# Kernel optimization log

Hardware: AMD Instinct MI355X
Metric: run time of the kernel (lower is better)

## Reference

```python
import jax, jax.numpy as jnp
import numpy as np

N_USERS = 50000
N_ENTITIES = 100000
N_FACTORS = 8
N_RELATIONS = 17  # weight has n_relations-1 = 16 rows
EMB = 64
N_EDGES = 2_000_000
NNZ = 2_000_000
SLOPE = 0.2


def setup_inputs() -> dict:
    key = jax.random.key(0)
    ks = jax.random.split(key, 16)
    inp = {
        "entity_emb": jax.random.normal(ks[0], (N_ENTITIES, EMB), jnp.float32),
        "user_emb": jax.random.normal(ks[1], (N_USERS, EMB), jnp.float32),
        "latent_emb": jax.random.normal(ks[2], (N_FACTORS, EMB), jnp.float32),
        "edge_index": jax.random.randint(ks[3], (2, N_EDGES), 0, N_ENTITIES, jnp.int32),
        "edge_type": jax.random.randint(ks[4], (N_EDGES,), 1, N_RELATIONS, jnp.int32),
        "interact_rows": jax.random.randint(ks[5], (NNZ,), 0, N_USERS, jnp.int32),
        "interact_cols": jax.random.randint(ks[6], (NNZ,), 0, N_ENTITIES, jnp.int32),
        "interact_vals": jax.random.uniform(ks[7], (NNZ,), jnp.float32),
        "weight": jax.random.normal(ks[8], (N_RELATIONS - 1, EMB), jnp.float32),
        "entity_cate_set": jax.random.randint(ks[9], (N_ENTITIES,), 1, 33, jnp.int32),
        # params (torch Linear convention: y = x @ W.T + b)
        "W_user_att": jax.random.normal(ks[10], (N_FACTORS, N_FACTORS), jnp.float32) * 0.1,
        "b_user_att": jnp.zeros((N_FACTORS,), jnp.float32),
        "W_weight_att": jax.random.normal(ks[11], (N_RELATIONS - 1, N_RELATIONS - 1), jnp.float32) * 0.1,
        "b_weight_att": jnp.zeros((N_RELATIONS - 1,), jnp.float32),
        "W1": jax.random.normal(ks[12], (EMB, EMB), jnp.float32) * 0.1,
        "b1": jnp.zeros((EMB,), jnp.float32),
        "W2": jax.random.normal(ks[13], (EMB, EMB), jnp.float32) * 0.1,
        "b2": jnp.zeros((EMB,), jnp.float32),
    }
    return inp


def _lin(x, W, b):
    return x @ W.T + b


def reference(entity_emb, user_emb, latent_emb, edge_index, edge_type,
              interact_rows, interact_cols, interact_vals, weight, entity_cate_set,
              W_user_att, b_user_att, W_weight_att, b_weight_att, W1, b1, W2, b2):
    head, tail = edge_index[0], edge_index[1]

    # KG aggregate: gather-multiply-scatter_mean (is_div=False branch)
    neigh = entity_emb[tail] * weight[edge_type - 1]            # [E, C]
    sums = jax.ops.segment_sum(neigh, head, num_segments=N_ENTITIES)
    cnt = jax.ops.segment_sum(jnp.ones((neigh.shape[0],), neigh.dtype),
                              head, num_segments=N_ENTITIES)
    entity_agg = sums / jnp.maximum(cnt, 1.0)[:, None]          # [N_ent, C]

    # user aggregate: sparse mm (COO) interact_mat @ entity_emb
    user_agg = jax.ops.segment_sum(interact_vals[:, None] * entity_emb[interact_cols],
                                   interact_rows, num_segments=N_USERS)  # [U, C]

    # user -> latent interest attention
    score_ = _lin(user_emb, W1, b1) @ _lin(latent_emb, W1, b1).T          # [U, F]
    score = jax.nn.softmax(jax.nn.leaky_relu(_lin(score_, W_user_att, b_user_att), SLOPE), axis=1)  # [U, F]

    score_rp = _lin(latent_emb, W2, b2) @ _lin(weight, W2, b2).T          # [F, R-1]
    latent_new = jax.nn.softmax(jax.nn.leaky_relu(_lin(score_rp, W_weight_att, b_weight_att), SLOPE), axis=-1) @ weight  # [F, C]

    # (disen_weight * score).sum(dim=1) == score @ latent_new
    user_agg = user_agg * (score @ latent_new) + user_agg
    return (entity_agg, user_agg, latent_new)
```

## Files before the change

kernel.cpp:

```cpp
#include <hip/hip_runtime.h>
#include <hip/hip_bf16.h>

#define N_USERS    50000
#define N_ENTITIES 100000
#define EMB        64
#define N_EDGES    2000000
#define NNZ        2000000
#define SLOPE      0.2f

#define KROWS   256
#define KSHIFT  8
#define NBK     391
#define UROWS   128
#define USHIFT  7
#define NBU     391
#define CAPK    8192
#define CAPU    7680
#define CHUNK   8192
#define PB      ((N_EDGES + CHUNK - 1) / CHUNK)

__global__ __launch_bounds__(512) void hist_both(const int* __restrict__ head,
                                                 const int* __restrict__ urows,
                                                 int* __restrict__ kgOffs,
                                                 int* __restrict__ uOffs) {
    __shared__ int lhk[NBK];
    __shared__ int lhu[NBU];
    int tid = threadIdx.x;
    for (int t = tid; t < NBK; t += 512) lhk[t] = 0;
    for (int t = tid; t < NBU; t += 512) lhu[t] = 0;
    __syncthreads();
    int base = blockIdx.x * CHUNK;
#pragma unroll 4
    for (int j = 0; j < CHUNK / 512; ++j) {
        int i = base + j * 512 + tid;
        if (i < N_EDGES) atomicAdd(&lhk[head[i] >> KSHIFT], 1);
        if (i < NNZ)     atomicAdd(&lhu[urows[i] >> USHIFT], 1);
    }
    __syncthreads();
    for (int t = tid; t < NBK; t += 512) { int c = lhk[t]; if (c) atomicAdd(&kgOffs[t], c); }
    for (int t = tid; t < NBU; t += 512) { int c = lhu[t]; if (c) atomicAdd(&uOffs[t], c); }
}

__global__ __launch_bounds__(512) void scan_both(int* __restrict__ kgOffs,
                                                 int* __restrict__ kgCur,
                                                 int* __restrict__ uOffs,
                                                 int* __restrict__ uCur) {
    __shared__ int tsum[512];
    int n     = (blockIdx.x == 0) ? NBK : NBU;
    int* offs = (blockIdx.x == 0) ? kgOffs : uOffs;
    int* cur  = (blockIdx.x == 0) ? kgCur  : uCur;
    int tid = threadIdx.x;
    int v = (tid < n) ? offs[tid] : 0;
    tsum[tid] = v;
    __syncthreads();
    for (int off = 1; off < 512; off <<= 1) {
        int t = (tid >= off) ? tsum[tid - off] : 0;
        __syncthreads();
        tsum[tid] += t;
        __syncthreads();
    }
    if (tid < n) { int e = tsum[tid] - v; offs[tid] = e; cur[tid] = e; }
    if (tid == n - 1) offs[n] = tsum[tid];
}

__global__ __launch_bounds__(512) void scatter_both(const int* __restrict__ head,
                                                    const int* __restrict__ tail,
                                                    const int* __restrict__ etype,
                                                    int* __restrict__ kgCur,
                                                    int* __restrict__ kgPay,
                                                    const int* __restrict__ urows,
                                                    const int* __restrict__ ucols,
                                                    const float* __restrict__ uvals,
                                                    int* __restrict__ uCur,
                                                    int2* __restrict__ uPay) {
    __shared__ int lh[NBK];
    __shared__ int lb[NBK];
    int tid = threadIdx.x;
    bool isKg = blockIdx.x < PB;
    int base = (isKg ? blockIdx.x : blockIdx.x - PB) * CHUNK;

    for (int t = tid; t < NBK; t += 512) lh[t] = 0;
    __syncthreads();
    if (isKg) {
#pragma unroll 4
        for (int j = 0; j < CHUNK / 512; ++j) {
            int i = base + j * 512 + tid;
            if (i < N_EDGES) atomicAdd(&lh[head[i] >> KSHIFT], 1);
        }
    } else {
#pragma unroll 4
        for (int j = 0; j < CHUNK / 512; ++j) {
            int i = base + j * 512 + tid;
            if (i < NNZ) atomicAdd(&lh[urows[i] >> USHIFT], 1);
        }
    }
    __syncthreads();
    int* cur = isKg ? kgCur : uCur;
    for (int t = tid; t < NBK; t += 512) {
        int c = lh[t];
        lb[t] = c ? atomicAdd(&cur[t], c) : 0;
        lh[t] = 0;
    }
    __syncthreads();
    if (isKg) {
#pragma unroll 4
        for (int j = 0; j < CHUNK / 512; ++j) {
            int i = base + j * 512 + tid;
            if (i < N_EDGES) {
                int h = head[i];
                int b = h >> KSHIFT;
                int p = lb[b] + atomicAdd(&lh[b], 1);
                kgPay[p] = tail[i] | ((etype[i] - 1) << 17) | ((h & (KROWS - 1)) << 21);
            }
        }
    } else {
#pragma unroll 4
        for (int j = 0; j < CHUNK / 512; ++j) {
            int i = base + j * 512 + tid;
            if (i < NNZ) {
                int r = urows[i];
                int b = r >> USHIFT;
                int p = lb[b] + atomicAdd(&lh[b], 1);
                uPay[p] = make_int2(ucols[i] | ((r & (UROWS - 1)) << 17),
                                    __float_as_int(uvals[i]));
            }
        }
    }
}

__global__ __launch_bounds__(1024, 8) void acc_both(
        const int* __restrict__ kgPay, const int* __restrict__ kgOffs,
        const int2* __restrict__ uPay, const int* __restrict__ uOffs,
        const float* __restrict__ entity_emb,
        const float* __restrict__ weight,
        const float* __restrict__ user_emb,
        const float* __restrict__ P,
        const float* __restrict__ cvec,
        const float* __restrict__ W_user_att,
        const float* __restrict__ b_user_att,
        const float* __restrict__ latent_new,
        float* __restrict__ ent_out,
        float* __restrict__ user_out) {
    __shared__ long long smem8[7873];
    int t = threadIdx.x, d = t & 63, wv = t >> 6;

    if (blockIdx.x < NBK) {
        int* spay = (int*)smem8;
        int* lcnt = spay + CAPK;
        int* lofs = lcnt + KROWS;
        int* sc   = lofs + KROWS + 1;
        int start = kgOffs[blockIdx.x], end = kgOffs[blockIdx.x + 1];
        int n = end - start; if (n > CAPK) n = CAPK;

        if (t < KROWS) lcnt[t] = 0;
        __syncthreads();
        for (int i = t; i < n; i += 1024)
            atomicAdd(&lcnt[(kgPay[start + i] >> 21) & (KROWS - 1)], 1);
        __syncthreads();
        if (t < KROWS) sc[t] = lcnt[t];
        __syncthreads();
        for (int off = 1; off < KROWS; off <<= 1) {
            int v = (t < KROWS && t >= off) ? sc[t - off] : 0;
            __syncthreads();
            if (t < KROWS) sc[t] += v;
            __syncthreads();
        }
        if (t < KROWS) { int e = sc[t] - lcnt[t]; lofs[t] = e; lcnt[t] = e; }
        if (t == 0) lofs[KROWS] = n;
        __syncthreads();
        for (int i = t; i < n; i += 1024) {
            int v = kgPay[start + i];
            int p = atomicAdd(&lcnt[(v >> 21) & (KROWS - 1)], 1);
            spay[p] = v;
        }
        __syncthreads();

        int rowbase = blockIdx.x * KROWS;
        for (int rr = 0; rr < KROWS / 16; ++rr) {
            int r = wv * (KROWS / 16) + rr;
            int gr = rowbase + r;
            if (gr >= N_ENTITIES) break;
            int s0 = lofs[r], e0 = lofs[r + 1];
            int cnt = e0 - s0;
            float acc = 0.f;
            int i = s0;
            for (; i + 7 < e0; i += 8) {
                float a0 = 0.f, a1 = 0.f;
#pragma unroll
                for (int u = 0; u < 8; u += 2) {
                    int va = spay[i + u], vb = spay[i + u + 1];
                    a0 += entity_emb[(va & 0x1FFFF) * EMB + d] * weight[((va >> 17) & 15) * EMB + d];
                    a1 += entity_emb[(vb & 0x1FFFF) * EMB + d] * weight[((vb >> 17) & 15) * EMB + d];
                }
                acc += a0 + a1;
            }
            for (; i < e0; ++i) {
                int v = spay[i];
                acc += entity_emb[(v & 0x1FFFF) * EMB + d] * weight[((v >> 17) & 15) * EMB + d];
            }
            for (int j = start + CAPK; j < end; ++j) {
                int v = kgPay[j];
                if (((v >> 21) & (KROWS - 1)) == r) {
                    acc += entity_emb[(v & 0x1FFFF) * EMB + d] * weight[((v >> 17) & 15) * EMB + d];
                    ++cnt;
                }
            }
            ent_out[gr * EMB + d] = acc / fmaxf((float)cnt, 1.f);
        }
    } else {
        int2* spay = (int2*)smem8;
        int* lcnt = (int*)(spay + CAPU);
        int* lofs = lcnt + UROWS;
        int* sc   = lofs + UROWS + 1;
        int bk = blockIdx.x - NBK;
        int start = uOffs[bk], end = uOffs[bk + 1];
        int n = end - start; if (n > CAPU) n = CAPU;

        if (t < UROWS) lcnt[t] = 0;
        __syncthreads();
        for (int i = t; i < n; i += 1024)
            atomicAdd(&lcnt[(uPay[start + i].x >> 17) & (UROWS - 1)], 1);
        __syncthreads();
        if (t < UROWS) sc[t] = lcnt[t];
        __syncthreads();
        for (int off = 1; off < UROWS; off <<= 1) {
            int v = (t < UROWS && t >= off) ? sc[t - off] : 0;
            __syncthreads();
            if (t < UROWS) sc[t] += v;
            __syncthreads();
        }
        if (t < UROWS) { int e = sc[t] - lcnt[t]; lofs[t] = e; lcnt[t] = e; }
        if (t == 0) lofs[UROWS] = n;
        __syncthreads();
        for (int i = t; i < n; i += 1024) {
            int2 v = uPay[start + i];
            int p = atomicAdd(&lcnt[(v.x >> 17) & (UROWS - 1)], 1);
            spay[p] = v;
        }
        __syncthreads();

        int rowbase = bk * UROWS;
        for (int rr = 0; rr < UROWS / 16; ++rr) {
            int r = wv * (UROWS / 16) + rr;
            int gr = rowbase + r;
            if (gr >= N_USERS) break;
            int s0 = lofs[r], e0 = lofs[r + 1];
            float acc = 0.f;
            int i = s0;
            for (; i + 7 < e0; i += 8) {
                float a0 = 0.f, a1 = 0.f;
#pragma unroll
                for (int u = 0; u < 8; u += 2) {
                    int2 va = spay[i + u], vb = spay[i + u + 1];
                    a0 += __int_as_float(va.y) * entity_emb[(va.x & 0x1FFFF) * EMB + d];
                    a1 += __int_as_float(vb.y) * entity_emb[(vb.x & 0x1FFFF) * EMB + d];
                }
                acc += a0 + a1;
            }
            for (; i < e0; ++i) {
                int2 v = spay[i];
                acc += __int_as_float(v.y) * entity_emb[(v.x & 0x1FFFF) * EMB + d];
            }
            for (int j = start + CAPU; j < end; ++j) {
                int2 v = uPay[j];
                if (((v.x >> 17) & (UROWS - 1)) == r)
                    acc += __int_as_float(v.y) * entity_emb[(v.x & 0x1FFFF) * EMB + d];
            }

            float ue = user_emb[gr * EMB + d];
            float s[8];
#pragma unroll
            for (int f = 0; f < 8; ++f) s[f] = ue * P[d * 8 + f];
#pragma unroll
            for (int off = 32; off; off >>= 1) {
#pragma unroll
                for (int f = 0; f < 8; ++f) s[f] += __shfl_xor(s[f], off, 64);
            }
#pragma unroll
            for (int f = 0; f < 8; ++f) s[f] += cvec[f];
            float att[8];
            float mx = -1e30f;
#pragma unroll
            for (int k = 0; k < 8; ++k) {
                float a = b_user_att[k];
#pragma unroll
                for (int j = 0; j < 8; ++j) a += s[j] * W_user_att[k * 8 + j];
                a = a > 0.f ? a : SLOPE * a;
                att[k] = a;
                mx = fmaxf(mx, a);
            }
            float sum = 0.f;
#pragma unroll
            for (int k = 0; k < 8; ++k) { att[k] = __expf(att[k] - mx); sum += att[k]; }
            float inv = 1.f / sum;
            float g = 0.f;
#pragma unroll
            for (int f = 0; f < 8; ++f) g += att[f] * inv * latent_new[f * EMB + d];
            user_out[gr * EMB + d] = acc * (1.f + g);
        }
    }
}

__global__ void small_dense(const float* __restrict__ latent_emb,
                            const float* __restrict__ weight,
                            const float* __restrict__ W_weight_att,
                            const float* __restrict__ b_weight_att,
                            const float* __restrict__ W1,
                            const float* __restrict__ b1,
                            const float* __restrict__ W2,
                            const float* __restrict__ b2,
                            float* __restrict__ P_out,
                            float* __restrict__ c_out,
                            float* __restrict__ latent_new_out) {
    __shared__ float lat1[8 * 64];
    __shared__ float lat2[8 * 64];
    __shared__ float wl2[16 * 64];
    __shared__ float srp[8 * 16];
    __shared__ float soft[8 * 16];
    int l = threadIdx.x;

    for (int f = 0; f < 8; ++f) {
        float a1 = b1[l], a2 = b2[l];
        for (int k = 0; k < 64; ++k) {
            float le = latent_emb[f * 64 + k];
            a1 += le * W1[l * 64 + k];
            a2 += le * W2[l * 64 + k];
        }
        lat1[f * 64 + l] = a1;
        lat2[f * 64 + l] = a2;
    }
    for (int r = 0; r < 16; ++r) {
        float a = b2[l];
        for (int k = 0; k < 64; ++k) a += weight[r * 64 + k] * W2[l * 64 + k];
        wl2[r * 64 + l] = a;
    }
    __syncthreads();

    for (int f = 0; f < 8; ++f) {
        float p = 0.f;
        for (int d = 0; d < 64; ++d) p += W1[d * 64 + l] * lat1[f * 64 + d];
        P_out[l * 8 + f] = p;
    }
    if (l < 8) {
        float cc = 0.f;
        for (int d = 0; d < 64; ++d) cc += b1[d] * lat1[l * 64 + d];
        c_out[l] = cc;
    }
    for (int idx = l; idx < 128; idx += 64) {
        int f = idx >> 4, r = idx & 15;
        float a = 0.f;
        for (int d = 0; d < 64; ++d) a += lat2[f * 64 + d] * wl2[r * 64 + d];
        srp[idx] = a;
    }
    __syncthreads();

    if (l < 8) {
        int f = l;
        float att[16];
        float mx = -1e30f;
        for (int k = 0; k < 16; ++k) {
            float a = b_weight_att[k];
            for (int j = 0; j < 16; ++j) a += srp[f * 16 + j] * W_weight_att[k * 16 + j];
            a = a > 0.f ? a : SLOPE * a;
            att[k] = a;
            mx = fmaxf(mx, a);
        }
        float s = 0.f;
        for (int k = 0; k < 16; ++k) { att[k] = expf(att[k] - mx); s += att[k]; }
        float inv = 1.f / s;
        for (int k = 0; k < 16; ++k) soft[f * 16 + k] = att[k] * inv;
    }
    __syncthreads();

    for (int f = 0; f < 8; ++f) {
        float a = 0.f;
        for (int r = 0; r < 16; ++r) a += soft[f * 16 + r] * weight[r * 64 + l];
        latent_new_out[f * 64 + l] = a;
    }
}

__global__ void kg_scatter(const int* __restrict__ head, const int* __restrict__ tail,
                           const int* __restrict__ etype,
                           const float* __restrict__ entity_emb,
                           const float* __restrict__ weight,
                           float* __restrict__ sums, float* __restrict__ cnt) {
    int gid = blockIdx.x * blockDim.x + threadIdx.x;
    int e = gid >> 6, d = threadIdx.x & 63;
    if (e >= N_EDGES) return;
    int h = head[e], t = tail[e], w = etype[e] - 1;
    float v = entity_emb[t * EMB + d] * weight[w * EMB + d];
    unsafeAtomicAdd(&sums[h * EMB + d], v);
    if (d == 0) unsafeAtomicAdd(&cnt[h], 1.0f);
}

__global__ void user_scatter(const int* __restrict__ rows, const int* __restrict__ cols,
                             const float* __restrict__ vals,
                             const float* __restrict__ entity_emb,
                             float* __restrict__ user_sums) {
    int gid = blockIdx.x * blockDim.x + threadIdx.x;
    int e = gid >> 6, d = threadIdx.x & 63;
    if (e >= NNZ) return;
    float v = vals[e] * entity_emb[cols[e] * EMB + d];
    unsafeAtomicAdd(&user_sums[rows[e] * EMB + d], v);
}

__global__ void entity_div(float* __restrict__ ent, const float* __restrict__ cnt) {
    int gid = blockIdx.x * blockDim.x + threadIdx.x;
    if (gid >= N_ENTITIES * EMB) return;
    float c = cnt[gid >> 6];
    ent[gid] = ent[gid] / fmaxf(c, 1.0f);
}

__global__ void user_finalize(const float* __restrict__ user_emb,
                              const float* __restrict__ P,
                              const float* __restrict__ c,
                              const float* __restrict__ W_user_att,
                              const float* __restrict__ b_user_att,
                              const float* __restrict__ latent_new,
                              float* __restrict__ user_out) {
    int gid = blockIdx.x * blockDim.x + threadIdx.x;
    int u = gid >> 6, lane = threadIdx.x & 63;
    if (u >= N_USERS) return;
    float ue = user_emb[u * 64 + lane];
    float s[8];
#pragma unroll
    for (int f = 0; f < 8; ++f) s[f] = ue * P[lane * 8 + f];
#pragma unroll
    for (int off = 32; off; off >>= 1)
#pragma unroll
        for (int f = 0; f < 8; ++f) s[f] += __shfl_xor(s[f], off, 64);
#pragma unroll
    for (int f = 0; f < 8; ++f) s[f] += c[f];
    float att[8], mx = -1e30f;
#pragma unroll
    for (int k = 0; k < 8; ++k) {
        float a = b_user_att[k];
#pragma unroll
        for (int j = 0; j < 8; ++j) a += s[j] * W_user_att[k * 8 + j];
        a = a > 0.f ? a : SLOPE * a;
        att[k] = a;
        mx = fmaxf(mx, a);
    }
    float sum = 0.f;
#pragma unroll
    for (int k = 0; k < 8; ++k) { att[k] = expf(att[k] - mx); sum += att[k]; }
    float inv = 1.f / sum, g = 0.f;
#pragma unroll
    for (int f = 0; f < 8; ++f) g += att[f] * inv * latent_new[f * 64 + lane];
    float ua = user_out[u * 64 + lane];
    user_out[u * 64 + lane] = ua * (1.f + g);
}

extern "C" void kernel_launch(void* const* d_in, const int* in_sizes, int n_in,
                              void* d_out, int out_size, void* d_ws, size_t ws_size,
                              hipStream_t stream) {
    const float* entity_emb   = (const float*)d_in[0];
    const float* user_emb     = (const float*)d_in[1];
    const float* latent_emb   = (const float*)d_in[2];
    const int*   edge_index   = (const int*)d_in[3];
    const int*   edge_type    = (const int*)d_in[4];
    const int*   irows        = (const int*)d_in[5];
    const int*   icols        = (const int*)d_in[6];
    const float* ivals        = (const float*)d_in[7];
    const float* weight       = (const float*)d_in[8];
    const float* W_user_att   = (const float*)d_in[10];
    const float* b_user_att   = (const float*)d_in[11];
    const float* W_weight_att = (const float*)d_in[12];
    const float* b_weight_att = (const float*)d_in[13];
    const float* W1           = (const float*)d_in[14];
    const float* b1           = (const float*)d_in[15];
    const float* W2           = (const float*)d_in[16];
    const float* b2           = (const float*)d_in[17];

    float* out      = (float*)d_out;
    float* ent_out  = out;
    float* user_out = out + (size_t)N_ENTITIES * EMB;
    float* lat_out  = user_out + (size_t)N_USERS * EMB;

    const int* head = edge_index;
    const int* tail = edge_index + N_EDGES;

    int* ws_i = (int*)d_ws;
    int*   kgOffs = ws_i;
    int*   uOffs  = kgOffs + (NBK + 1);
    int*   kgCur  = uOffs + (NBU + 1);
    int*   uCur   = kgCur + NBK;
    int*   kgPay  = uCur + NBU;
    int2*  uPay   = (int2*)(kgPay + N_EDGES);
    float* Pbuf   = (float*)(uPay + NNZ);
    float* cbuf   = Pbuf + 64 * 8;
    size_t need_bytes = (size_t)((NBK + 1) + (NBU + 1) + NBK + NBU +
                                 N_EDGES + 2 * (size_t)NNZ + 512 + 8) * 4;

    if (ws_size >= need_bytes) {
        hipMemsetAsync(kgOffs, 0, (size_t)((NBK + 1) + (NBU + 1)) * sizeof(int), stream);

        hist_both<<<PB, 512, 0, stream>>>(head, irows, kgOffs, uOffs);
        scan_both<<<2, 512, 0, stream>>>(kgOffs, kgCur, uOffs, uCur);
        scatter_both<<<2 * PB, 512, 0, stream>>>(head, tail, edge_type, kgCur, kgPay,
                                                 irows, icols, ivals, uCur, uPay);
        small_dense<<<1, 64, 0, stream>>>(latent_emb, weight, W_weight_att,
                                          b_weight_att, W1, b1, W2, b2,
                                          Pbuf, cbuf, lat_out);
        acc_both<<<NBK + NBU, 1024, 0, stream>>>(kgPay, kgOffs, uPay, uOffs,
                                                 entity_emb, weight, user_emb,
                                                 Pbuf, cbuf, W_user_att, b_user_att,
                                                 lat_out, ent_out, user_out);
    } else {
        float* cnt   = (float*)d_ws;
        float* Pbuf2 = cnt + N_ENTITIES;
        float* cbuf2 = Pbuf2 + 64 * 8;
        hipMemsetAsync(ent_out, 0,
                       (size_t)(N_ENTITIES + N_USERS) * EMB * sizeof(float), stream);
        hipMemsetAsync(cnt, 0, N_ENTITIES * sizeof(float), stream);
        int blocks_edges = (N_EDGES * 64) / 256;
        kg_scatter<<<blocks_edges, 256, 0, stream>>>(head, tail, edge_type, entity_emb,
                                                     weight, ent_out, cnt);
        user_scatter<<<blocks_edges, 256, 0, stream>>>(irows, icols, ivals, entity_emb,
                                                       user_out);
        small_dense<<<1, 64, 0, stream>>>(latent_emb, weight, W_weight_att,
                                          b_weight_att, W1, b1, W2, b2,
                                          Pbuf2, cbuf2, lat_out);
        user_finalize<<<(N_USERS * 64) / 256, 256, 0, stream>>>(user_emb, Pbuf2, cbuf2,
                                                                W_user_att, b_user_att,
                                                                lat_out, user_out);
        entity_div<<<(N_ENTITIES * EMB) / 256, 256, 0, stream>>>(ent_out, cnt);
    }
}
```

Before: 442.4 us.

## Accumulate bucketed rows in shared-memory atomics instead of per-row local sort

```diff
diff --git a/kernel.cpp b/kernel.cpp
--- a/kernel.cpp
+++ b/kernel.cpp
@@ -1,5 +1,4 @@
 #include <hip/hip_runtime.h>
-#include <hip/hip_bf16.h>
 
 #define N_USERS    50000
 #define N_ENTITIES 100000
@@ -8,15 +7,12 @@
 #define NNZ        2000000
 #define SLOPE      0.2f
 
-#define KROWS   256
-#define KSHIFT  8
-#define NBK     391
-#define UROWS   128
-#define USHIFT  7
+#define RSHIFT  7
+#define BROWS   128
+#define NBK     782
 #define NBU     391
-#define CAPK    8192
-#define CAPU    7680
 #define CHUNK   8192
+#define EPT     (CHUNK / 512)
 #define PB      ((N_EDGES + CHUNK - 1) / CHUNK)
 
 __global__ __launch_bounds__(512) void hist_both(const int* __restrict__ head,
@@ -31,21 +27,21 @@
     __syncthreads();
     int base = blockIdx.x * CHUNK;
 #pragma unroll 4
-    for (int j = 0; j < CHUNK / 512; ++j) {
+    for (int j = 0; j < EPT; ++j) {
         int i = base + j * 512 + tid;
-        if (i < N_EDGES) atomicAdd(&lhk[head[i] >> KSHIFT], 1);
-        if (i < NNZ)     atomicAdd(&lhu[urows[i] >> USHIFT], 1);
+        if (i < N_EDGES) atomicAdd(&lhk[head[i] >> RSHIFT], 1);
+        if (i < NNZ)     atomicAdd(&lhu[urows[i] >> RSHIFT], 1);
     }
     __syncthreads();
     for (int t = tid; t < NBK; t += 512) { int c = lhk[t]; if (c) atomicAdd(&kgOffs[t], c); }
     for (int t = tid; t < NBU; t += 512) { int c = lhu[t]; if (c) atomicAdd(&uOffs[t], c); }
 }
 
-__global__ __launch_bounds__(512) void scan_both(int* __restrict__ kgOffs,
-                                                 int* __restrict__ kgCur,
-                                                 int* __restrict__ uOffs,
-                                                 int* __restrict__ uCur) {
-    __shared__ int tsum[512];
+__global__ __launch_bounds__(1024) void scan_both(int* __restrict__ kgOffs,
+                                                  int* __restrict__ kgCur,
+                                                  int* __restrict__ uOffs,
+                                                  int* __restrict__ uCur) {
+    __shared__ int tsum[1024];
     int n     = (blockIdx.x == 0) ? NBK : NBU;
     int* offs = (blockIdx.x == 0) ? kgOffs : uOffs;
     int* cur  = (blockIdx.x == 0) ? kgCur  : uCur;
@@ -53,7 +49,7 @@
     int v = (tid < n) ? offs[tid] : 0;
     tsum[tid] = v;
     __syncthreads();
-    for (int off = 1; off < 512; off <<= 1) {
+    for (int off = 1; off < 1024; off <<= 1) {
         int t = (tid >= off) ? tsum[tid - off] : 0;
         __syncthreads();
         tsum[tid] += t;
@@ -61,6 +57,105 @@
     }
     if (tid < n) { int e = tsum[tid] - v; offs[tid] = e; cur[tid] = e; }
     if (tid == n - 1) offs[n] = tsum[tid];
+}
+
+__device__ void small_dense_body(int l,
+                                 const float* __restrict__ latent_emb,
+                                 const float* __restrict__ weight,
+                                 const float* __restrict__ W_weight_att,
+                                 const float* __restrict__ b_weight_att,
+                                 const float* __restrict__ W1,
+                                 const float* __restrict__ b1,
+                                 const float* __restrict__ W2,
+                                 const float* __restrict__ b2,
+                                 float* __restrict__ P_out,
+                                 float* __restrict__ c_out,
+                                 float* __restrict__ latent_new_out) {
+    __shared__ float lat1[8 * 64];
+    __shared__ float lat2[8 * 64];
+    __shared__ float wl2[16 * 64];
+    __shared__ float srp[8 * 16];
+    __shared__ float soft[8 * 16];
+
+    if (l < 64) {
+        for (int f = 0; f < 8; ++f) {
+            float a1 = b1[l], a2 = b2[l];
+            for (int k = 0; k < 64; ++k) {
+                float le = latent_emb[f * 64 + k];
+                a1 += le * W1[l * 64 + k];
+                a2 += le * W2[l * 64 + k];
+            }
+            lat1[f * 64 + l] = a1;
+            lat2[f * 64 + l] = a2;
+        }
+        for (int r = 0; r < 16; ++r) {
+            float a = b2[l];
+            for (int k = 0; k < 64; ++k) a += weight[r * 64 + k] * W2[l * 64 + k];
+            wl2[r * 64 + l] = a;
+        }
+    }
+    __syncthreads();
+
+    if (l < 64) {
+        for (int f = 0; f < 8; ++f) {
+            float p = 0.f;
+            for (int d = 0; d < 64; ++d) p += W1[d * 64 + l] * lat1[f * 64 + d];
+            P_out[l * 8 + f] = p;
+        }
+        if (l < 8) {
+            float cc = 0.f;
+            for (int d = 0; d < 64; ++d) cc += b1[d] * lat1[l * 64 + d];
+            c_out[l] = cc;
+        }
+        for (int idx = l; idx < 128; idx += 64) {
+            int f = idx >> 4, r = idx & 15;
+            float a = 0.f;
+            for (int d = 0; d < 64; ++d) a += lat2[f * 64 + d] * wl2[r * 64 + d];
+            srp[idx] = a;
+        }
+    }
+    __syncthreads();
+
+    if (l < 8) {
+        int f = l;
+        float att[16];
+        float mx = -1e30f;
+        for (int k = 0; k < 16; ++k) {
+            float a = b_weight_att[k];
+            for (int j = 0; j < 16; ++j) a += srp[f * 16 + j] * W_weight_att[k * 16 + j];
+            a = a > 0.f ? a : SLOPE * a;
+            att[k] = a;
+            mx = fmaxf(mx, a);
+        }
+        float s = 0.f;
+        for (int k = 0; k < 16; ++k) { att[k] = expf(att[k] - mx); s += att[k]; }
+        float inv = 1.f / s;
+        for (int k = 0; k < 16; ++k) soft[f * 16 + k] = att[k] * inv;
+    }
+    __syncthreads();
+
+    if (l < 64) {
+        for (int f = 0; f < 8; ++f) {
+            float a = 0.f;
+            for (int r = 0; r < 16; ++r) a += soft[f * 16 + r] * weight[r * 64 + l];
+            latent_new_out[f * 64 + l] = a;
+        }
+    }
+}
+
+__global__ void small_dense(const float* __restrict__ latent_emb,
+                            const float* __restrict__ weight,
+                            const float* __restrict__ W_weight_att,
+                            const float* __restrict__ b_weight_att,
+                            const float* __restrict__ W1,
+                            const float* __restrict__ b1,
+                            const float* __restrict__ W2,
+                            const float* __restrict__ b2,
+                            float* __restrict__ P_out,
+                            float* __restrict__ c_out,
+                            float* __restrict__ latent_new_out) {
+    small_dense_body(threadIdx.x, latent_emb, weight, W_weight_att, b_weight_att,
+                     W1, b1, W2, b2, P_out, c_out, latent_new_out);
 }
 
 __global__ __launch_bounds__(512) void scatter_both(const int* __restrict__ head,
@@ -72,56 +167,72 @@
                                                     const int* __restrict__ ucols,
                                                     const float* __restrict__ uvals,
                                                     int* __restrict__ uCur,
-                                                    int2* __restrict__ uPay) {
+                                                    int2* __restrict__ uPay,
+                                                    const float* __restrict__ latent_emb,
+                                                    const float* __restrict__ weight,
+                                                    const float* __restrict__ W_weight_att,
+                                                    const float* __restrict__ b_weight_att,
+                                                    const float* __restrict__ W1,
+                                                    const float* __restrict__ b1,
+                                                    const float* __restrict__ W2,
+                                                    const float* __restrict__ b2,
+                                                    float* __restrict__ Pbuf,
+                                                    float* __restrict__ cbuf,
+                                                    float* __restrict__ lat_out) {
+    if (blockIdx.x == 2 * PB) {
+        small_dense_body(threadIdx.x, latent_emb, weight, W_weight_att,
+                         b_weight_att, W1, b1, W2, b2, Pbuf, cbuf, lat_out);
+        return;
+    }
+
     __shared__ int lh[NBK];
     __shared__ int lb[NBK];
     int tid = threadIdx.x;
     bool isKg = blockIdx.x < PB;
     int base = (isKg ? blockIdx.x : blockIdx.x - PB) * CHUNK;
+    int nb   = isKg ? NBK : NBU;
+    int nTot = isKg ? N_EDGES : NNZ;
+    const int* src = isKg ? head : urows;
+    int* cur = isKg ? kgCur : uCur;
 
     for (int t = tid; t < NBK; t += 512) lh[t] = 0;
     __syncthreads();
-    if (isKg) {
-#pragma unroll 4
-        for (int j = 0; j < CHUNK / 512; ++j) {
-            int i = base + j * 512 + tid;
-            if (i < N_EDGES) atomicAdd(&lh[head[i] >> KSHIFT], 1);
-        }
-    } else {
-#pragma unroll 4
-        for (int j = 0; j < CHUNK / 512; ++j) {
-            int i = base + j * 512 + tid;
-            if (i < NNZ) atomicAdd(&lh[urows[i] >> USHIFT], 1);
-        }
-    }
-    __syncthreads();
-    int* cur = isKg ? kgCur : uCur;
-    for (int t = tid; t < NBK; t += 512) {
+
+    int hreg[EPT];
+#pragma unroll
+    for (int j = 0; j < EPT; ++j) {
+        int i = base + j * 512 + tid;
+        int h = (i < nTot) ? src[i] : -1;
+        hreg[j] = h;
+        if (h >= 0) atomicAdd(&lh[h >> RSHIFT], 1);
+    }
+    __syncthreads();
+    for (int t = tid; t < nb; t += 512) {
         int c = lh[t];
         lb[t] = c ? atomicAdd(&cur[t], c) : 0;
         lh[t] = 0;
     }
     __syncthreads();
     if (isKg) {
-#pragma unroll 4
-        for (int j = 0; j < CHUNK / 512; ++j) {
-            int i = base + j * 512 + tid;
-            if (i < N_EDGES) {
-                int h = head[i];
-                int b = h >> KSHIFT;
+#pragma unroll
+        for (int j = 0; j < EPT; ++j) {
+            int h = hreg[j];
+            if (h >= 0) {
+                int i = base + j * 512 + tid;
+                int b = h >> RSHIFT;
                 int p = lb[b] + atomicAdd(&lh[b], 1);
-                kgPay[p] = tail[i] | ((etype[i] - 1) << 17) | ((h & (KROWS - 1)) << 21);
+                kgPay[p] = tail[i] | ((etype[i] - 1) << 17) | ((h & (BROWS - 1)) << 21);
             }
         }
     } else {
-#pragma unroll 4
-        for (int j = 0; j < CHUNK / 512; ++j) {
-            int i = base + j * 512 + tid;
-            if (i < NNZ) {
-                int r = urows[i];
-                int b = r >> USHIFT;
+#pragma unroll
+        for (int j = 0; j < EPT; ++j) {
+            int h = hreg[j];
+            if (h >= 0) {
+                int i = base + j * 512 + tid;
+                int b = h >> RSHIFT;
                 int p = lb[b] + atomicAdd(&lh[b], 1);
-                uPay[p] = make_int2(ucols[i] | ((r & (UROWS - 1)) << 17),
+                uPay[p] = make_int2(ucols[i] | ((h & (BROWS - 1)) << 17),
                                     __float_as_int(uvals[i]));
             }
         }
@@ -141,136 +252,54 @@
         const float* __restrict__ latent_new,
         float* __restrict__ ent_out,
         float* __restrict__ user_out) {
-    __shared__ long long smem8[7873];
-    int t = threadIdx.x, d = t & 63, wv = t >> 6;
-
-    if (blockIdx.x < NBK) {
-        int* spay = (int*)smem8;
-        int* lcnt = spay + CAPK;
-        int* lofs = lcnt + KROWS;
-        int* sc   = lofs + KROWS + 1;
-        int start = kgOffs[blockIdx.x], end = kgOffs[blockIdx.x + 1];
-        int n = end - start; if (n > CAPK) n = CAPK;
-
-        if (t < KROWS) lcnt[t] = 0;
+    __shared__ float accum[BROWS * EMB];
+    __shared__ int   lcnt[BROWS];
+    int t  = threadIdx.x;
+    int wv = t >> 6, l = t & 63;
+    int h  = l >> 5, dd = l & 31;
+    int lane2 = (wv << 1) + h;
+
+    float4* a4 = (float4*)accum;
+    a4[t]        = make_float4(0.f, 0.f, 0.f, 0.f);
+    a4[t + 1024] = make_float4(0.f, 0.f, 0.f, 0.f);
+    if (t < BROWS) lcnt[t] = 0;
+    __syncthreads();
+
+    const float2* e2 = (const float2*)entity_emb;
+
+    if (blockIdx.x < NBU) {
+        int bk = blockIdx.x;
+        int start = uOffs[bk], n = uOffs[bk + 1] - start;
+        const int2* pay = uPay + start;
+        int nIt = (n + 31) >> 5;
+#pragma unroll 2
+        for (int it = 0; it < nIt; ++it) {
+            int ie = (it << 5) + lane2;
+            if (ie < n) {
+                int2 v = pay[ie];
+                int col = v.x & 0x1FFFF;
+                int r   = (v.x >> 17) & (BROWS - 1);
+                float val = __int_as_float(v.y);
+                float2 e = e2[(col << 5) + dd];
+                float p0 = val * e.x, p1 = val * e.y;
+                int wb = (r << 6) + (dd << 1);
+                atomicAdd(&accum[wb + h],       h ? p1 : p0);
+                atomicAdd(&accum[wb + (1 ^ h)], h ? p0 : p1);
+            }
+        }
         __syncthreads();
-        for (int i = t; i < n; i += 1024)
-            atomicAdd(&lcnt[(kgPay[start + i] >> 21) & (KROWS - 1)], 1);
-        __syncthreads();
-        if (t < KROWS) sc[t] = lcnt[t];
-        __syncthreads();
-        for (int off = 1; off < KROWS; off <<= 1) {
-            int v = (t < KROWS && t >= off) ? sc[t - off] : 0;
-            __syncthreads();
-            if (t < KROWS) sc[t] += v;
-            __syncthreads();
-        }
-        if (t < KROWS) { int e = sc[t] - lcnt[t]; lofs[t] = e; lcnt[t] = e; }
-        if (t == 0) lofs[KROWS] = n;
-        __syncthreads();
-        for (int i = t; i < n; i += 1024) {
-            int v = kgPay[start + i];
-            int p = atomicAdd(&lcnt[(v >> 21) & (KROWS - 1)], 1);
-            spay[p] = v;
-        }
-        __syncthreads();
-
-        int rowbase = blockIdx.x * KROWS;
-        for (int rr = 0; rr < KROWS / 16; ++rr) {
-            int r = wv * (KROWS / 16) + rr;
-            int gr = rowbase + r;
-            if (gr >= N_ENTITIES) break;
-            int s0 = lofs[r], e0 = lofs[r + 1];
-            int cnt = e0 - s0;
-            float acc = 0.f;
-            int i = s0;
-            for (; i + 7 < e0; i += 8) {
-                float a0 = 0.f, a1 = 0.f;
-#pragma unroll
-                for (int u = 0; u < 8; u += 2) {
-                    int va = spay[i + u], vb = spay[i + u + 1];
-                    a0 += entity_emb[(va & 0x1FFFF) * EMB + d] * weight[((va >> 17) & 15) * EMB + d];
-                    a1 += entity_emb[(vb & 0x1FFFF) * EMB + d] * weight[((vb >> 17) & 15) * EMB + d];
-                }
-                acc += a0 + a1;
-            }
-            for (; i < e0; ++i) {
-                int v = spay[i];
-                acc += entity_emb[(v & 0x1FFFF) * EMB + d] * weight[((v >> 17) & 15) * EMB + d];
-            }
-            for (int j = start + CAPK; j < end; ++j) {
-                int v = kgPay[j];
-                if (((v >> 21) & (KROWS - 1)) == r) {
-                    acc += entity_emb[(v & 0x1FFFF) * EMB + d] * weight[((v >> 17) & 15) * EMB + d];
-                    ++cnt;
-                }
-            }
-            ent_out[gr * EMB + d] = acc / fmaxf((float)cnt, 1.f);
-        }
-    } else {
-        int2* spay = (int2*)smem8;
-        int* lcnt = (int*)(spay + CAPU);
-        int* lofs = lcnt + UROWS;
-        int* sc   = lofs + UROWS + 1;
-        int bk = blockIdx.x - NBK;
-        int start = uOffs[bk], end = uOffs[bk + 1];
-        int n = end - start; if (n > CAPU) n = CAPU;
-
-        if (t < UROWS) lcnt[t] = 0;
-        __syncthreads();
-        for (int i = t; i < n; i += 1024)
-            atomicAdd(&lcnt[(uPay[start + i].x >> 17) & (UROWS - 1)], 1);
-        __syncthreads();
-        if (t < UROWS) sc[t] = lcnt[t];
-        __syncthreads();
-        for (int off = 1; off < UROWS; off <<= 1) {
-            int v = (t < UROWS && t >= off) ? sc[t - off] : 0;
-            __syncthreads();
-            if (t < UROWS) sc[t] += v;
-            __syncthreads();
-        }
-        if (t < UROWS) { int e = sc[t] - lcnt[t]; lofs[t] = e; lcnt[t] = e; }
-        if (t == 0) lofs[UROWS] = n;
-        __syncthreads();
-        for (int i = t; i < n; i += 1024) {
-            int2 v = uPay[start + i];
-            int p = atomicAdd(&lcnt[(v.x >> 17) & (UROWS - 1)], 1);
-            spay[p] = v;
-        }
-        __syncthreads();
-
-        int rowbase = bk * UROWS;
-        for (int rr = 0; rr < UROWS / 16; ++rr) {
-            int r = wv * (UROWS / 16) + rr;
+
+        int rowbase = bk * BROWS;
+        for (int k = 0; k < BROWS / 16; ++k) {
+            int r = (k << 4) + wv;
             int gr = rowbase + r;
             if (gr >= N_USERS) break;
-            int s0 = lofs[r], e0 = lofs[r + 1];
-            float acc = 0.f;
-            int i = s0;
-            for (; i + 7 < e0; i += 8) {
-                float a0 = 0.f, a1 = 0.f;
-#pragma unroll
-                for (int u = 0; u < 8; u += 2) {
-                    int2 va = spay[i + u], vb = spay[i + u + 1];
-                    a0 += __int_as_float(va.y) * entity_emb[(va.x & 0x1FFFF) * EMB + d];
-                    a1 += __int_as_float(vb.y) * entity_emb[(vb.x & 0x1FFFF) * EMB + d];
-                }
-                acc += a0 + a1;
-            }
-            for (; i < e0; ++i) {
-                int2 v = spay[i];
-                acc += __int_as_float(v.y) * entity_emb[(v.x & 0x1FFFF) * EMB + d];
-            }
-            for (int j = start + CAPU; j < end; ++j) {
-                int2 v = uPay[j];
-                if (((v.x >> 17) & (UROWS - 1)) == r)
-                    acc += __int_as_float(v.y) * entity_emb[(v.x & 0x1FFFF) * EMB + d];
-            }
-
-            float ue = user_emb[gr * EMB + d];
+            float acc = accum[(r << 6) + l];
+
+            float ue = user_emb[(size_t)gr * EMB + l];
             float s[8];
 #pragma unroll
-            for (int f = 0; f < 8; ++f) s[f] = ue * P[d * 8 + f];
+            for (int f = 0; f < 8; ++f) s[f] = ue * P[l * 8 + f];
 #pragma unroll
             for (int off = 32; off; off >>= 1) {
 #pragma unroll
@@ -281,101 +310,56 @@
             float att[8];
             float mx = -1e30f;
 #pragma unroll
-            for (int k = 0; k < 8; ++k) {
-                float a = b_user_att[k];
-#pragma unroll
-                for (int j = 0; j < 8; ++j) a += s[j] * W_user_att[k * 8 + j];
+            for (int q = 0; q < 8; ++q) {
+                float a = b_user_att[q];
+#pragma unroll
+                for (int j = 0; j < 8; ++j) a += s[j] * W_user_att[q * 8 + j];
                 a = a > 0.f ? a : SLOPE * a;
-                att[k] = a;
+                att[q] = a;
                 mx = fmaxf(mx, a);
             }
             float sum = 0.f;
 #pragma unroll
-            for (int k = 0; k < 8; ++k) { att[k] = __expf(att[k] - mx); sum += att[k]; }
+            for (int q = 0; q < 8; ++q) { att[q] = __expf(att[q] - mx); sum += att[q]; }
             float inv = 1.f / sum;
             float g = 0.f;
 #pragma unroll
-            for (int f = 0; f < 8; ++f) g += att[f] * inv * latent_new[f * EMB + d];
-            user_out[gr * EMB + d] = acc * (1.f + g);
-        }
-    }
-}
-
-__global__ void small_dense(const float* __restrict__ latent_emb,
-                            const float* __restrict__ weight,
-                            const float* __restrict__ W_weight_att,
-                            const float* __restrict__ b_weight_att,
-                            const float* __restrict__ W1,
-                            const float* __restrict__ b1,
-                            const float* __restrict__ W2,
-                            const float* __restrict__ b2,
-                            float* __restrict__ P_out,
-                            float* __restrict__ c_out,
-                            float* __restrict__ latent_new_out) {
-    __shared__ float lat1[8 * 64];
-    __shared__ float lat2[8 * 64];
-    __shared__ float wl2[16 * 64];
-    __shared__ float srp[8 * 16];
-    __shared__ float soft[8 * 16];
-    int l = threadIdx.x;
-
-    for (int f = 0; f < 8; ++f) {
-        float a1 = b1[l], a2 = b2[l];
-        for (int k = 0; k < 64; ++k) {
-            float le = latent_emb[f * 64 + k];
-            a1 += le * W1[l * 64 + k];
-            a2 += le * W2[l * 64 + k];
-        }
-        lat1[f * 64 + l] = a1;
-        lat2[f * 64 + l] = a2;
-    }
-    for (int r = 0; r < 16; ++r) {
-        float a = b2[l];
-        for (int k = 0; k < 64; ++k) a += weight[r * 64 + k] * W2[l * 64 + k];
-        wl2[r * 64 + l] = a;
-    }
-    __syncthreads();
-
-    for (int f = 0; f < 8; ++f) {
-        float p = 0.f;
-        for (int d = 0; d < 64; ++d) p += W1[d * 64 + l] * lat1[f * 64 + d];
-        P_out[l * 8 + f] = p;
-    }
-    if (l < 8) {
-        float cc = 0.f;
-        for (int d = 0; d < 64; ++d) cc += b1[d] * lat1[l * 64 + d];
-        c_out[l] = cc;
-    }
-    for (int idx = l; idx < 128; idx += 64) {
-        int f = idx >> 4, r = idx & 15;
-        float a = 0.f;
-        for (int d = 0; d < 64; ++d) a += lat2[f * 64 + d] * wl2[r * 64 + d];
-        srp[idx] = a;
-    }
-    __syncthreads();
-
-    if (l < 8) {
-        int f = l;
-        float att[16];
-        float mx = -1e30f;
-        for (int k = 0; k < 16; ++k) {
-            float a = b_weight_att[k];
-            for (int j = 0; j < 16; ++j) a += srp[f * 16 + j] * W_weight_att[k * 16 + j];
-            a = a > 0.f ? a : SLOPE * a;
-            att[k] = a;
-            mx = fmaxf(mx, a);
-        }
-        float s = 0.f;
-        for (int k = 0; k < 16; ++k) { att[k] = expf(att[k] - mx); s += att[k]; }
-        float inv = 1.f / s;
-        for (int k = 0; k < 16; ++k) soft[f * 16 + k] = att[k] * inv;
-    }
-    __syncthreads();
-
-    for (int f = 0; f < 8; ++f) {
-        float a = 0.f;
-        for (int r = 0; r < 16; ++r) a += soft[f * 16 + r] * weight[r * 64 + l];
-        latent_new_out[f * 64 + l] = a;
+            for (int f = 0; f < 8; ++f) g += att[f] * inv * latent_new[f * EMB + l];
+            user_out[(size_t)gr * EMB + l] = acc * (1.f + g);
+        }
+    } else {
+        int bk = blockIdx.x - NBU;
+        int start = kgOffs[bk], n = kgOffs[bk + 1] - start;
+        const int* pay = kgPay + start;
+        int nIt = (n + 31) >> 5;
+#pragma unroll 2
+        for (int it = 0; it < nIt; ++it) {
+            int ie = (it << 5) + lane2;
+            if (ie < n) {
+                int v  = pay[ie];
+                int tl = v & 0x1FFFF;
+                int w  = (v >> 17) & 15;
+                int r  = (v >> 21) & (BROWS - 1);
+                float2 e  = e2[(tl << 5) + dd];
+                float2 wt = *((const float2*)weight + ((w << 5) + dd));
+                float p0 = e.x * wt.x, p1 = e.y * wt.y;
+                int wb = (r << 6) + (dd << 1);
+                atomicAdd(&accum[wb + h],       h ? p1 : p0);
+                atomicAdd(&accum[wb + (1 ^ h)], h ? p0 : p1);
+                if (dd == 0) atomicAdd(&lcnt[r], 1);
+            }
+        }
+        __syncthreads();
+
+        int rowbase = bk * BROWS;
+#pragma unroll
+        for (int k = 0; k < BROWS / 16; ++k) {
+            int r = (k << 4) + wv;
+            int gr = rowbase + r;
+            if (gr < N_ENTITIES)
+                ent_out[(size_t)gr * EMB + l] =
+                    accum[(r << 6) + l] / fmaxf((float)lcnt[r], 1.f);
+        }
     }
 }
 
@@ -496,12 +480,12 @@
         hipMemsetAsync(kgOffs, 0, (size_t)((NBK + 1) + (NBU + 1)) * sizeof(int), stream);
 
         hist_both<<<PB, 512, 0, stream>>>(head, irows, kgOffs, uOffs);
-        scan_both<<<2, 512, 0, stream>>>(kgOffs, kgCur, uOffs, uCur);
-        scatter_both<<<2 * PB, 512, 0, stream>>>(head, tail, edge_type, kgCur, kgPay,
-                                                 irows, icols, ivals, uCur, uPay);
-        small_dense<<<1, 64, 0, stream>>>(latent_emb, weight, W_weight_att,
-                                          b_weight_att, W1, b1, W2, b2,
-                                          Pbuf, cbuf, lat_out);
+        scan_both<<<2, 1024, 0, stream>>>(kgOffs, kgCur, uOffs, uCur);
+        scatter_both<<<2 * PB + 1, 512, 0, stream>>>(head, tail, edge_type, kgCur, kgPay,
+                                                     irows, icols, ivals, uCur, uPay,
+                                                     latent_emb, weight, W_weight_att,
+                                                     b_weight_att, W1, b1, W2, b2,
+                                                     Pbuf, cbuf, lat_out);
         acc_both<<<NBK + NBU, 1024, 0, stream>>>(kgPay, kgOffs, uPay, uOffs,
                                                  entity_emb, weight, user_emb,
                                                  Pbuf, cbuf, W_user_att, b_user_att,
```

New measurement: 1.738 ms. +292.9%, slower.
